# Optimization experiments

Measured on AMD Instinct MI355X. Metric: run time of the kernel, lower is better.

## Reference

```python
import jax, jax.numpy as jnp
import numpy as np

N, E, FEAT, H, C = 50000, 800000, 256, 256, 64
THETA = 0.5


def _l2norm(x, eps=1e-12):
    n = jnp.sqrt(jnp.sum(x * x, axis=-1, keepdims=True))
    return x / jnp.maximum(n, eps)


def _gcn_conv(x, row, col, W, b):
    # x: [N, Fin]; row/col: [E+N] (self loops already appended); all edge weights are 1
    n = x.shape[0]
    h = x @ W                                                   # [N, Fout]
    ones = jnp.ones(row.shape, dtype=h.dtype)
    deg = jax.ops.segment_sum(ones, row, num_segments=n)        # in-degree over rows
    deg_safe = jnp.where(deg > 0, deg, 1.0)
    dinv = jnp.where(deg > 0, jax.lax.rsqrt(deg_safe), 0.0)
    norm = dinv[row] * dinv[col]                                # [E+N]
    msg = norm[:, None] * h[col]                                # gather + weight
    out = jax.ops.segment_sum(msg, row, num_segments=n)         # scatter-add
    return out + b


def setup_inputs() -> dict:
    key = jax.random.key(0)
    ks = jax.random.split(key, 10)
    edge_index = jax.random.randint(ks[0], (2, E), 0, N, dtype=jnp.int32)
    neg_edge_index = jax.random.randint(ks[1], (2, E), 0, N, dtype=jnp.int32)
    features = jax.random.normal(ks[2], (N, FEAT), dtype=jnp.float32)
    label_smoothing = jax.random.uniform(ks[3], (E,), dtype=jnp.float32)
    W1 = jax.random.normal(ks[4], (FEAT, H), dtype=jnp.float32) / np.sqrt(FEAT)
    b1 = jnp.zeros((H,), dtype=jnp.float32)
    W2 = jax.random.normal(ks[5], (H, H), dtype=jnp.float32) / np.sqrt(H)
    b2 = jnp.zeros((H,), dtype=jnp.float32)
    Wy = jax.random.normal(ks[6], (H, C), dtype=jnp.float32) / np.sqrt(H)
    by = jnp.zeros((C,), dtype=jnp.float32)
    return {"edge_index": edge_index, "features": features,
            "label_smoothing": label_smoothing, "neg_edge_index": neg_edge_index,
            "W1": W1, "b1": b1, "W2": W2, "b2": b2, "Wy": Wy, "by": by}


def reference(edge_index, features, label_smoothing, neg_edge_index,
              W1, b1, W2, b2, Wy, by):
    n = features.shape[0]
    self_idx = jnp.arange(n, dtype=edge_index.dtype)
    row = jnp.concatenate([edge_index[0], self_idx])
    col = jnp.concatenate([edge_index[1], self_idx])

    # GCN (dropout=0.0)
    x1 = jax.nn.relu(_gcn_conv(features, row, col, W1, b1))
    x2 = _gcn_conv(x1, row, col, W2, b2)
    rep = _l2norm(x2)
    rep = _l2norm(rep)  # second normalize in q_phi1.forward
    y = rep @ Wy + by

    # reconstruct_loss (i<j filtering done via static-shape masks)
    e0, e1 = edge_index[0], edge_index[1]
    n0, n1 = neg_edge_index[0], neg_edge_index[1]
    pos_mask = (e0 < e1).astype(rep.dtype)
    neg_mask = (n0 < n1).astype(rep.dtype)

    neg_w = jax.nn.relu(jnp.sum(rep[n0] * rep[n1], axis=1))
    pos_w = jax.nn.relu(jnp.sum(rep[e0] * rep[e1], axis=1))
    pos_fsim = jnp.sum(features[e0] * features[e1], axis=1)
    pos = pos_fsim * THETA + pos_w * (1.0 - THETA)

    n_pos = jnp.sum(pos_mask)
    n_neg = jnp.sum(neg_mask)
    neg_loss = jnp.sum(neg_mask * neg_w * neg_w)
    pos_loss = jnp.sum(pos_mask * (pos - label_smoothing) ** 2)
    rec_loss = (neg_loss + pos_loss) * n / (n_neg + n_pos)
    return rep, rec_loss, y
```

## Files before the change

### kernel.cpp

```cpp
#include <hip/hip_runtime.h>
#include <hip/hip_bf16.h>

#define FEAT 256
#define HDIM 256
#define CDIM 64
#define THETA 0.5f
#define APAD 264

typedef float floatx2 __attribute__((ext_vector_type(2)));
typedef __attribute__((ext_vector_type(8))) short bf16x8;
typedef __attribute__((ext_vector_type(4))) float f32x4;

__global__ __launch_bounds__(256) void deg_count(const int* __restrict__ e0, int E, int* deg) {
    int i = blockIdx.x * 256 + threadIdx.x;
    if (i < E) atomicAdd(&deg[e0[i]], 1);
}

__global__ __launch_bounds__(256) void make_dinv(const int* __restrict__ deg, float* __restrict__ dinv, int N) {
    int i = blockIdx.x * 256 + threadIdx.x;
    if (i < N) dinv[i] = rsqrtf((float)(deg[i] + 1));
}

__global__ __launch_bounds__(256) void scan1(const int* __restrict__ deg,
                                             int* __restrict__ rowptr,
                                             int* __restrict__ blkS, int N) {
    __shared__ int sh[256];
    const int tid = threadIdx.x;
    const int i = blockIdx.x * 256 + tid;
    int v = (i < N) ? deg[i] : 0;
    sh[tid] = v;
    __syncthreads();
#pragma unroll
    for (int off = 1; off < 256; off <<= 1) {
        int t = (tid >= off) ? sh[tid - off] : 0;
        __syncthreads();
        sh[tid] += t;
        __syncthreads();
    }
    if (i < N) rowptr[i] = sh[tid] - v;
    if (tid == 255) blkS[blockIdx.x] = sh[255];
}

__global__ __launch_bounds__(256) void scan2(int* __restrict__ blkS, int nb) {
    __shared__ int part[256];
    const int tid = threadIdx.x;
    const int chunk = (nb + 255) / 256;
    const int s = tid * chunk;
    const int e = min(s + chunk, nb);
    int sum = 0;
    for (int i = s; i < e; ++i) sum += blkS[i];
    part[tid] = sum;
    __syncthreads();
#pragma unroll
    for (int off = 1; off < 256; off <<= 1) {
        int t = (tid >= off) ? part[tid - off] : 0;
        __syncthreads();
        part[tid] += t;
        __syncthreads();
    }
    int run = part[tid] - sum;
    for (int i = s; i < e; ++i) {
        int v = blkS[i];
        blkS[i] = run;
        run += v;
    }
}

__global__ __launch_bounds__(256) void scan3(int* __restrict__ rowptr,
                                             int* __restrict__ cursor,
                                             const int* __restrict__ blkS, int N, int E) {
    const int i = blockIdx.x * 256 + threadIdx.x;
    if (i < N) {
        int v = rowptr[i] + blkS[blockIdx.x];
        rowptr[i] = v;
        cursor[i] = v;
    }
    if (i == 0) rowptr[N] = E;
}

__global__ __launch_bounds__(256) void bucket_edges(const int* __restrict__ e0,
                                                    const int* __restrict__ e1,
                                                    int* cursor, int* __restrict__ colIdx, int E) {
    int i = blockIdx.x * 256 + threadIdx.x;
    if (i < E) {
        int r = e0[i];
        int pos = atomicAdd(&cursor[r], 1);
        colIdx[pos] = e1[i];
    }
}

__device__ __forceinline__ unsigned short f2bf(float f) {
    unsigned int u = __float_as_uint(f);
    u += 0x7fffu + ((u >> 16) & 1u);
    return (unsigned short)(u >> 16);
}
__device__ __forceinline__ float bfl(unsigned int u) { return __uint_as_float(u << 16); }
__device__ __forceinline__ float bfh(unsigned int u) { return __uint_as_float(u & 0xffff0000u); }
__device__ __forceinline__ unsigned char f2f8(float f) {
    int w = __builtin_amdgcn_cvt_pk_fp8_f32(f, f, 0, false);
    return (unsigned char)(w & 0xff);
}

__global__ __launch_bounds__(256) void to_fp8(const float* __restrict__ src,
                                              unsigned char* __restrict__ dst, int n8) {
    int i = blockIdx.x * 256 + threadIdx.x;
    if (i >= n8) return;
    float4 a = ((const float4*)src)[2 * i];
    float4 b = ((const float4*)src)[2 * i + 1];
    int w0 = __builtin_amdgcn_cvt_pk_fp8_f32(a.x, a.y, 0, false);
    w0 = __builtin_amdgcn_cvt_pk_fp8_f32(a.z, a.w, w0, true);
    int w1 = __builtin_amdgcn_cvt_pk_fp8_f32(b.x, b.y, 0, false);
    w1 = __builtin_amdgcn_cvt_pk_fp8_f32(b.z, b.w, w1, true);
    uint2 o;
    o.x = (unsigned int)w0;
    o.y = (unsigned int)w1;
    ((uint2*)dst)[i] = o;
}

__global__ __launch_bounds__(256) void transposeW(const float* __restrict__ W,
                                                  unsigned short* __restrict__ Wt) {
    int k = blockIdx.x;
    int n = threadIdx.x;
    Wt[(size_t)n * 256 + k] = f2bf(W[(size_t)k * 256 + n]);
}

__global__ __launch_bounds__(64) void transposeWy(const float* __restrict__ W,
                                                  unsigned short* __restrict__ Wt) {
    int k = blockIdx.x;
    int n = threadIdx.x;
    Wt[(size_t)n * 256 + k] = f2bf(W[(size_t)k * 64 + n]);
}

__device__ __forceinline__ void gemm_core_f8out(const unsigned short* Al,
                                                const unsigned short* __restrict__ Wt,
                                                unsigned char* __restrict__ out,
                                                int m0, int wv, int lane, int M) {
    f32x4 acc[4][4] = {};
    const int r16 = lane & 15;
    const int kg8 = (lane >> 4) * 8;
    const unsigned short* wbase = Wt + ((size_t)(wv * 64 + r16)) * 256 + kg8;
    const unsigned short* abase = Al + r16 * APAD + kg8;

#pragma unroll
    for (int k0 = 0; k0 < 256; k0 += 32) {
        bf16x8 af[4], bfr[4];
#pragma unroll
        for (int mi = 0; mi < 4; ++mi)
            af[mi] = *(const bf16x8*)&abase[mi * 16 * APAD + k0];
#pragma unroll
        for (int ni = 0; ni < 4; ++ni)
            bfr[ni] = *(const bf16x8*)&wbase[ni * 16 * 256 + k0];
#pragma unroll
        for (int mi = 0; mi < 4; ++mi)
#pragma unroll
            for (int ni = 0; ni < 4; ++ni)
                acc[mi][ni] = __builtin_amdgcn_mfma_f32_16x16x32_bf16(af[mi], bfr[ni], acc[mi][ni], 0, 0, 0);
    }

#pragma unroll
    for (int mi = 0; mi < 4; ++mi) {
        int rbase = m0 + mi * 16 + ((lane >> 4) << 2);
#pragma unroll
        for (int ni = 0; ni < 4; ++ni) {
            int col = (wv << 6) + (ni << 4) + (lane & 15);
#pragma unroll
            for (int j = 0; j < 4; ++j) {
                int row = rbase + j;
                if (row < M) out[(size_t)row * 256 + col] = f2f8(acc[mi][ni][j]);
            }
        }
    }
}

__global__ __launch_bounds__(256) void gemm_mfma_f32A(const float* __restrict__ A,
                                                      const unsigned short* __restrict__ Wt,
                                                      unsigned char* __restrict__ out, int M) {
    __shared__ unsigned short Al[64 * APAD];
    const int tid = threadIdx.x;
    const int m0 = blockIdx.x * 64;
#pragma unroll
    for (int i = 0; i < 8; ++i) {
        int u = i * 256 + tid;
        int r = u >> 5;
        int c8 = (u & 31) * 8;
        int row = m0 + r;
        float4 v0, v1;
        if (row < M) {
            v0 = *(const float4*)&A[(size_t)row * 256 + c8];
            v1 = *(const float4*)&A[(size_t)row * 256 + c8 + 4];
        } else {
            v0 = make_float4(0.f, 0.f, 0.f, 0.f);
            v1 = v0;
        }
        uint4 o;
        o.x = (unsigned int)f2bf(v0.x) | ((unsigned int)f2bf(v0.y) << 16);
        o.y = (unsigned int)f2bf(v0.z) | ((unsigned int)f2bf(v0.w) << 16);
        o.z = (unsigned int)f2bf(v1.x) | ((unsigned int)f2bf(v1.y) << 16);
        o.w = (unsigned int)f2bf(v1.z) | ((unsigned int)f2bf(v1.w) << 16);
        *(uint4*)&Al[r * APAD + c8] = o;
    }
    __syncthreads();
    gemm_core_f8out(Al, Wt, out, m0, tid >> 6, tid & 63, M);
}

__global__ __launch_bounds__(256) void gemm_mfma_b16A(const unsigned short* __restrict__ A,
                                                      const unsigned short* __restrict__ Wt,
                                                      unsigned char* __restrict__ out, int M) {
    __shared__ unsigned short Al[64 * APAD];
    const int tid = threadIdx.x;
    const int m0 = blockIdx.x * 64;
#pragma unroll
    for (int i = 0; i < 8; ++i) {
        int u = i * 256 + tid;
        int r = u >> 5;
        int c8 = (u & 31) * 8;
        int row = m0 + r;
        uint4 o = make_uint4(0, 0, 0, 0);
        if (row < M) o = *(const uint4*)&A[(size_t)row * 256 + c8];
        *(uint4*)&Al[r * APAD + c8] = o;
    }
    __syncthreads();
    gemm_core_f8out(Al, Wt, out, m0, tid >> 6, tid & 63, M);
}

__global__ __launch_bounds__(256) void gemm_wy_mfma(const float* __restrict__ A,
                                                    const unsigned short* __restrict__ WyT,
                                                    const float* __restrict__ bias,
                                                    float* __restrict__ out, int M) {
    __shared__ unsigned short Al[64 * APAD];
    const int tid = threadIdx.x;
    const int m0 = blockIdx.x * 64;
    const int wv = tid >> 6;
    const int lane = tid & 63;

#pragma unroll
    for (int i = 0; i < 8; ++i) {
        int u = i * 256 + tid;
        int r = u >> 5;
        int c8 = (u & 31) * 8;
        int row = m0 + r;
        float4 v0, v1;
        if (row < M) {
            v0 = *(const float4*)&A[(size_t)row * 256 + c8];
            v1 = *(const float4*)&A[(size_t)row * 256 + c8 + 4];
        } else {
            v0 = make_float4(0.f, 0.f, 0.f, 0.f);
            v1 = v0;
        }
        uint4 o;
        o.x = (unsigned int)f2bf(v0.x) | ((unsigned int)f2bf(v0.y) << 16);
        o.y = (unsigned int)f2bf(v0.z) | ((unsigned int)f2bf(v0.w) << 16);
        o.z = (unsigned int)f2bf(v1.x) | ((unsigned int)f2bf(v1.y) << 16);
        o.w = (unsigned int)f2bf(v1.z) | ((unsigned int)f2bf(v1.w) << 16);
        *(uint4*)&Al[r * APAD + c8] = o;
    }
    __syncthreads();

    f32x4 acc[4] = {};
    const int r16 = lane & 15;
    const int kg8 = (lane >> 4) * 8;
    const unsigned short* wbase = WyT + ((size_t)(wv * 16 + r16)) * 256 + kg8;
    const unsigned short* abase = Al + r16 * APAD + kg8;

#pragma unroll
    for (int k0 = 0; k0 < 256; k0 += 32) {
        bf16x8 bfr = *(const bf16x8*)&wbase[k0];
#pragma unroll
        for (int mi = 0; mi < 4; ++mi) {
            bf16x8 af = *(const bf16x8*)&abase[mi * 16 * APAD + k0];
            acc[mi] = __builtin_amdgcn_mfma_f32_16x16x32_bf16(af, bfr, acc[mi], 0, 0, 0);
        }
    }

    int col = (wv << 4) + (lane & 15);
    float bv = bias[col];
#pragma unroll
    for (int mi = 0; mi < 4; ++mi) {
        int rbase = m0 + mi * 16 + ((lane >> 4) << 2);
#pragma unroll
        for (int j = 0; j < 4; ++j) {
            int row = rbase + j;
            if (row < M) out[(size_t)row * 64 + col] = acc[mi][j] + bv;
        }
    }
}

template <int DO_NORM>
__global__ __launch_bounds__(256) void spmm_gather_f8(const int* __restrict__ rowptr,
                                                      const int* __restrict__ colIdx,
                                                      const unsigned char* __restrict__ h8,
                                                      const float* __restrict__ dinv,
                                                      const float* __restrict__ bias,
                                                      unsigned short* __restrict__ out_b16,
                                                      float* __restrict__ rep,
                                                      unsigned char* __restrict__ rep8,
                                                      int N) {
    int row = (blockIdx.x * 256 + threadIdx.x) >> 6;
    int lane = threadIdx.x & 63;
    if (row >= N) return;
    int beg = rowptr[row];
    int end = rowptr[row + 1];
    float4 acc = make_float4(0.f, 0.f, 0.f, 0.f);
    int j = beg;
    for (; j + 7 < end; j += 8) {
        int cc[8];
#pragma unroll
        for (int q = 0; q < 8; ++q) cc[q] = colIdx[j + q];
        float ww[8];
#pragma unroll
        for (int q = 0; q < 8; ++q) ww[q] = dinv[cc[q]];
        unsigned int uu[8];
#pragma unroll
        for (int q = 0; q < 8; ++q) uu[q] = *(const unsigned int*)&h8[(size_t)cc[q] * 256 + lane * 4];
#pragma unroll
        for (int q = 0; q < 8; ++q) {
            floatx2 lo = __builtin_amdgcn_cvt_pk_f32_fp8((int)uu[q], false);
            floatx2 hi = __builtin_amdgcn_cvt_pk_f32_fp8((int)uu[q], true);
            acc.x = fmaf(ww[q], lo.x, acc.x); acc.y = fmaf(ww[q], lo.y, acc.y);
            acc.z = fmaf(ww[q], hi.x, acc.z); acc.w = fmaf(ww[q], hi.y, acc.w);
        }
    }
    for (; j < end; ++j) {
        int c = colIdx[j];
        float w = dinv[c];
        unsigned int u = *(const unsigned int*)&h8[(size_t)c * 256 + lane * 4];
        floatx2 lo = __builtin_amdgcn_cvt_pk_f32_fp8((int)u, false);
        floatx2 hi = __builtin_amdgcn_cvt_pk_f32_fp8((int)u, true);
        acc.x = fmaf(w, lo.x, acc.x); acc.y = fmaf(w, lo.y, acc.y);
        acc.z = fmaf(w, hi.x, acc.z); acc.w = fmaf(w, hi.y, acc.w);
    }
    float di = dinv[row];
    float s = di * di;
    unsigned int us = *(const unsigned int*)&h8[(size_t)row * 256 + lane * 4];
    floatx2 slo = __builtin_amdgcn_cvt_pk_f32_fp8((int)us, false);
    floatx2 shi = __builtin_amdgcn_cvt_pk_f32_fp8((int)us, true);
    float4 bv = *(const float4*)&bias[lane * 4];
    float4 r;
    r.x = fmaf(di, acc.x, fmaf(s, slo.x, bv.x));
    r.y = fmaf(di, acc.y, fmaf(s, slo.y, bv.y));
    r.z = fmaf(di, acc.z, fmaf(s, shi.x, bv.z));
    r.w = fmaf(di, acc.w, fmaf(s, shi.y, bv.w));
    if (DO_NORM == 0) {
        r.x = fmaxf(r.x, 0.f);
        r.y = fmaxf(r.y, 0.f);
        r.z = fmaxf(r.z, 0.f);
        r.w = fmaxf(r.w, 0.f);
        uint2 o;
        o.x = (unsigned int)f2bf(r.x) | ((unsigned int)f2bf(r.y) << 16);
        o.y = (unsigned int)f2bf(r.z) | ((unsigned int)f2bf(r.w) << 16);
        *(uint2*)&out_b16[(size_t)row * 256 + lane * 4] = o;
    } else {
        float ss = r.x * r.x + r.y * r.y + r.z * r.z + r.w * r.w;
#pragma unroll
        for (int o = 1; o < 64; o <<= 1) ss += __shfl_xor(ss, o);
        float inv = 1.0f / fmaxf(sqrtf(ss), 1e-12f);
        r.x *= inv; r.y *= inv; r.z *= inv; r.w *= inv;
        float ss2 = r.x * r.x + r.y * r.y + r.z * r.z + r.w * r.w;
#pragma unroll
        for (int o = 1; o < 64; o <<= 1) ss2 += __shfl_xor(ss2, o);
        float inv2 = 1.0f / fmaxf(sqrtf(ss2), 1e-12f);
        r.x *= inv2; r.y *= inv2; r.z *= inv2; r.w *= inv2;
        *(float4*)&rep[(size_t)row * 256 + lane * 4] = r;
        int w = __builtin_amdgcn_cvt_pk_fp8_f32(r.x, r.y, 0, false);
        w = __builtin_amdgcn_cvt_pk_fp8_f32(r.z, r.w, w, true);
        *(unsigned int*)&rep8[(size_t)row * 256 + lane * 4] = (unsigned int)w;
    }
}

__global__ __launch_bounds__(256) void count_blocks(const int* __restrict__ e0,
                                                    const int* __restrict__ e1,
                                                    const int* __restrict__ n0,
                                                    const int* __restrict__ n1,
                                                    int* __restrict__ blkP,
                                                    int* __restrict__ blkN, int E) {
    const int i = blockIdx.x * 256 + threadIdx.x;
    const int lane = threadIdx.x & 63;
    const int w = threadIdx.x >> 6;
    bool vp = false, vn = false;
    if (i < E) {
        vp = e0[i] < e1[i];
        vn = n0[i] < n1[i];
    }
    unsigned long long mp = __ballot(vp);
    unsigned long long mn = __ballot(vn);
    __shared__ int s[8];
    if (lane == 0) {
        s[w] = __popcll(mp);
        s[4 + w] = __popcll(mn);
    }
    __syncthreads();
    if (threadIdx.x == 0) blkP[blockIdx.x] = s[0] + s[1] + s[2] + s[3];
    if (threadIdx.x == 1) blkN[blockIdx.x] = s[4] + s[5] + s[6] + s[7];
}

__global__ __launch_bounds__(256) void scan_blocks(int* __restrict__ blkP, int* __restrict__ blkN,
                                                   int* __restrict__ cnt, int nb) {
    __shared__ int partP[256], partN[256];
    const int tid = threadIdx.x;
    const int chunk = (nb + 255) / 256;
    const int s = tid * chunk;
    const int e = min(s + chunk, nb);
    int sp = 0, sn = 0;
    for (int i = s; i < e; ++i) { sp += blkP[i]; sn += blkN[i]; }
    partP[tid] = sp;
    partN[tid] = sn;
    __syncthreads();
#pragma unroll
    for (int off = 1; off < 256; off <<= 1) {
        int tp = (tid >= off) ? partP[tid - off] : 0;
        int tn = (tid >= off) ? partN[tid - off] : 0;
        __syncthreads();
        partP[tid] += tp;
        partN[tid] += tn;
        __syncthreads();
    }
    int runP = partP[tid] - sp;
    int runN = partN[tid] - sn;
    for (int i = s; i < e; ++i) {
        int vp = blkP[i], vn = blkN[i];
        blkP[i] = runP;
        blkN[i] = runN;
        runP += vp;
        runN += vn;
    }
    if (tid == 255) { cnt[0] = runP; cnt[1] = runN; }
}

__global__ __launch_bounds__(256) void scatter_edges(const int* __restrict__ e0,
                                                     const int* __restrict__ e1,
                                                     const int* __restrict__ n0,
                                                     const int* __restrict__ n1,
                                                     const float* __restrict__ ls,
                                                     const int* __restrict__ blkP,
                                                     const int* __restrict__ blkN,
                                                     int2* __restrict__ posAB,
                                                     float* __restrict__ posLS,
                                                     int2* __restrict__ negCD, int E) {
    const int i = blockIdx.x * 256 + threadIdx.x;
    const int lane = threadIdx.x & 63;
    const int w = threadIdx.x >> 6;
    const unsigned long long below = (lane == 0) ? 0ull : ((1ull << lane) - 1ull);
    int a = 0, b = 0, c = 0, d = 0;
    float lsv = 0.f;
    bool vp = false, vn = false;
    if (i < E) {
        a = e0[i]; b = e1[i];
        c = n0[i]; d = n1[i];
        vp = a < b;
        vn = c < d;
        if (vp) lsv = ls[i];
    }
    unsigned long long mp = __ballot(vp);
    unsigned long long mn = __ballot(vn);
    __shared__ int sP[4], sN[4];
    if (lane == 0) {
        sP[w] = __popcll(mp);
        sN[w] = __popcll(mn);
    }
    __syncthreads();
    int baseP = blkP[blockIdx.x];
    int baseN = blkN[blockIdx.x];
    for (int q = 0; q < 4; ++q) {
        if (q < w) { baseP += sP[q]; baseN += sN[q]; }
    }
    if (vp) {
        int ofs = __popcll(mp & below);
        posAB[baseP + ofs] = make_int2(a, b);
        posLS[baseP + ofs] = lsv;
    }
    if (vn) {
        int ofs = __popcll(mn & below);
        negCD[baseN + ofs] = make_int2(c, d);
    }
}

__device__ __forceinline__ float dot16fp8(uint4 x, uint4 y) {
    float s = 0.f;
    const unsigned int xs[4] = {x.x, x.y, x.z, x.w};
    const unsigned int ys[4] = {y.x, y.y, y.z, y.w};
#pragma unroll
    for (int i = 0; i < 4; ++i) {
        floatx2 xl = __builtin_amdgcn_cvt_pk_f32_fp8((int)xs[i], false);
        floatx2 xh = __builtin_amdgcn_cvt_pk_f32_fp8((int)xs[i], true);
        floatx2 yl = __builtin_amdgcn_cvt_pk_f32_fp8((int)ys[i], false);
        floatx2 yh = __builtin_amdgcn_cvt_pk_f32_fp8((int)ys[i], true);
        s += xl.x * yl.x + xl.y * yl.y + xh.x * yh.x + xh.y * yh.y;
    }
    return s;
}

__global__ __launch_bounds__(256) void loss_pos(const int2* __restrict__ posAB,
                                                const float* __restrict__ posLS,
                                                const int* __restrict__ cnt,
                                                const unsigned char* __restrict__ rep8,
                                                const unsigned char* __restrict__ feat8,
                                                float* accum) {
    const int tid = threadIdx.x;
    const int l8 = tid & 7;
    const int grp = (blockIdx.x * 256 + tid) >> 3;
    const int ngrp = gridDim.x * 32;
    const int P = cnt[0];
    float ap = 0.f;
    for (int e = grp; e < P; e += ngrp) {
        int2 ab = posAB[e];
        const uint4* pra = (const uint4*)&rep8[(size_t)ab.x * 256 + l8 * 32];
        const uint4* prb = (const uint4*)&rep8[(size_t)ab.y * 256 + l8 * 32];
        const uint4* pfa = (const uint4*)&feat8[(size_t)ab.x * 256 + l8 * 32];
        const uint4* pfb = (const uint4*)&feat8[(size_t)ab.y * 256 + l8 * 32];
        uint4 ra0 = pra[0], ra1 = pra[1];
        uint4 rb0 = prb[0], rb1 = prb[1];
        uint4 fa0 = pfa[0], fa1 = pfa[1];
        uint4 fb0 = pfb[0], fb1 = pfb[1];
        float dp = dot16fp8(ra0, rb0) + dot16fp8(ra1, rb1);
        float df = dot16fp8(fa0, fb0) + dot16fp8(fa1, fb1);
#pragma unroll
        for (int o = 1; o < 8; o <<= 1) {
            dp += __shfl_xor(dp, o);
            df += __shfl_xor(df, o);
        }
        if (l8 == 0) {
            float pw = fmaxf(dp, 0.f);
            float pos = THETA * df + (1.0f - THETA) * pw;
            float t = pos - posLS[e];
            ap += t * t;
        }
    }
#pragma unroll
    for (int o = 1; o < 64; o <<= 1) ap += __shfl_xor(ap, o);
    __shared__ float s[4];
    if ((tid & 63) == 0) s[tid >> 6] = ap;
    __syncthreads();
    if (tid == 0) unsafeAtomicAdd(&accum[0], s[0] + s[1] + s[2] + s[3]);
}

__global__ __launch_bounds__(256) void loss_neg(const int2* __restrict__ negCD,
                                                const int* __restrict__ cnt,
                                                const unsigned char* __restrict__ rep8,
                                                float* accum) {
    const int tid = threadIdx.x;
    const int l8 = tid & 7;
    const int grp = (blockIdx.x * 256 + tid) >> 3;
    const int ngrp = gridDim.x * 32;
    const int Q = cnt[1];
    float an = 0.f;
    for (int e = grp; e < Q; e += ngrp) {
        int2 cd = negCD[e];
        const uint4* prc = (const uint4*)&rep8[(size_t)cd.x * 256 + l8 * 32];
        const uint4* prd = (const uint4*)&rep8[(size_t)cd.y * 256 + l8 * 32];
        uint4 rc0 = prc[0], rc1 = prc[1];
        uint4 rd0 = prd[0], rd1 = prd[1];
        float dn = dot16fp8(rc0, rd0) + dot16fp8(rc1, rd1);
#pragma unroll
        for (int o = 1; o < 8; o <<= 1) dn += __shfl_xor(dn, o);
        if (l8 == 0) {
            float nwt = fmaxf(dn, 0.f);
            an += nwt * nwt;
        }
    }
#pragma unroll
    for (int o = 1; o < 64; o <<= 1) an += __shfl_xor(an, o);
    __shared__ float s[4];
    if ((tid & 63) == 0) s[tid >> 6] = an;
    __syncthreads();
    if (tid == 0) unsafeAtomicAdd(&accum[1], s[0] + s[1] + s[2] + s[3]);
}

__global__ void loss_final(const float* __restrict__ accum, const int* __restrict__ cnt,
                           float* __restrict__ out, int N) {
    out[0] = (accum[0] + accum[1]) * (float)N / (float)(cnt[0] + cnt[1]);
}

extern "C" void kernel_launch(void* const* d_in, const int* in_sizes, int n_in,
                              void* d_out, int out_size, void* d_ws, size_t ws_size,
                              hipStream_t stream) {
    const int* edge = (const int*)d_in[0];
    const float* features = (const float*)d_in[1];
    const float* ls = (const float*)d_in[2];
    const int* nedge = (const int*)d_in[3];
    const float* W1 = (const float*)d_in[4];
    const float* b1 = (const float*)d_in[5];
    const float* W2 = (const float*)d_in[6];
    const float* b2 = (const float*)d_in[7];
    const float* Wy = (const float*)d_in[8];
    const float* by = (const float*)d_in[9];

    const int E = in_sizes[0] / 2;
    const int N = in_sizes[1] / FEAT;
    const int* e0 = edge;
    const int* e1 = edge + E;
    const int* n0 = nedge;
    const int* n1 = nedge + E;

    float* rep = (float*)d_out;
    float* rec = rep + (size_t)N * 256;
    float* y = rec + 1;

    char* base = (char*)d_ws;
    size_t off = 0;
    auto carve = [&](size_t bytes) -> void* {
        void* p = base + off;
        off += (bytes + 1023) & ~(size_t)1023;
        return p;
    };
    int* deg = (int*)carve((size_t)N * 4);
    float* dinv = (float*)carve((size_t)N * 4);
    float* accum = (float*)carve(16);
    int* cnt = (int*)carve(16);
    int* rowptr = (int*)carve((size_t)(N + 1) * 4);
    int* cursor = (int*)carve((size_t)N * 4);
    int* colIdx = (int*)carve((size_t)E * 4);
    unsigned char* h8 = (unsigned char*)carve((size_t)N * 256);
    unsigned short* x1B = (unsigned short*)carve((size_t)N * 256 * 2);
    unsigned char* feat8 = (unsigned char*)carve((size_t)N * 256);
    unsigned char* rep8 = (unsigned char*)carve((size_t)N * 256);
    unsigned short* Wt1 = (unsigned short*)carve(256 * 256 * 2);
    unsigned short* Wt2 = (unsigned short*)carve(256 * 256 * 2);
    unsigned short* WyT = (unsigned short*)carve(64 * 256 * 2);
    int2* posAB = (int2*)carve((size_t)E * 8);
    float* posLS = (float*)carve((size_t)E * 4);
    int2* negCD = (int2*)carve((size_t)E * 8);
    const int nb = (E + 255) / 256;
    int* blkP = (int*)carve((size_t)nb * 4);
    int* blkN = (int*)carve((size_t)nb * 4);
    const int nbn = (N + 255) / 256;
    int* blkS = (int*)carve((size_t)nbn * 4);

    hipMemsetAsync(deg, 0, (size_t)N * 4, stream);
    hipMemsetAsync(accum, 0, 16, stream);
    deg_count<<<(E + 255) / 256, 256, 0, stream>>>(e0, E, deg);
    make_dinv<<<(N + 255) / 256, 256, 0, stream>>>(deg, dinv, N);
    scan1<<<nbn, 256, 0, stream>>>(deg, rowptr, blkS, N);
    scan2<<<1, 256, 0, stream>>>(blkS, nbn);
    scan3<<<nbn, 256, 0, stream>>>(rowptr, cursor, blkS, N, E);
    bucket_edges<<<(E + 255) / 256, 256, 0, stream>>>(e0, e1, cursor, colIdx, E);

    count_blocks<<<nb, 256, 0, stream>>>(e0, e1, n0, n1, blkP, blkN, E);
    scan_blocks<<<1, 256, 0, stream>>>(blkP, blkN, cnt, nb);
    scatter_edges<<<nb, 256, 0, stream>>>(e0, e1, n0, n1, ls, blkP, blkN, posAB, posLS, negCD, E);

    const int gblk = (N + 63) / 64;
    const int wblk = (N + 3) / 4;
    const int n8 = N * 256 / 8;

    to_fp8<<<(n8 + 255) / 256, 256, 0, stream>>>(features, feat8, n8);
    transposeW<<<256, 256, 0, stream>>>(W1, Wt1);
    transposeW<<<256, 256, 0, stream>>>(W2, Wt2);
    transposeWy<<<256, 64, 0, stream>>>(Wy, WyT);

    gemm_mfma_f32A<<<gblk, 256, 0, stream>>>(features, Wt1, h8, N);
    spmm_gather_f8<0><<<wblk, 256, 0, stream>>>(rowptr, colIdx, h8, dinv, b1, x1B, nullptr, nullptr, N);

    gemm_mfma_b16A<<<gblk, 256, 0, stream>>>(x1B, Wt2, h8, N);
    spmm_gather_f8<1><<<wblk, 256, 0, stream>>>(rowptr, colIdx, h8, dinv, b2, nullptr, rep, rep8, N);

    gemm_wy_mfma<<<gblk, 256, 0, stream>>>(rep, WyT, by, y, N);

    loss_pos<<<2048, 256, 0, stream>>>(posAB, posLS, cnt, rep8, feat8, accum);
    loss_neg<<<2048, 256, 0, stream>>>(negCD, cnt, rep8, accum);
    loss_final<<<1, 1, 0, stream>>>(accum, cnt, rec, N);
}
```

Before: 405.5 us.

## Fuse preprocessing launches, merge loss kernels, read fp8 rep in Wy GEMM

```diff
diff --git a/kernel.cpp b/kernel.cpp
--- a/kernel.cpp
+++ b/kernel.cpp
@@ -11,23 +11,84 @@
 typedef __attribute__((ext_vector_type(8))) short bf16x8;
 typedef __attribute__((ext_vector_type(4))) float f32x4;
 
-__global__ __launch_bounds__(256) void deg_count(const int* __restrict__ e0, int E, int* deg) {
-    int i = blockIdx.x * 256 + threadIdx.x;
-    if (i < E) atomicAdd(&deg[e0[i]], 1);
-}
-
-__global__ __launch_bounds__(256) void make_dinv(const int* __restrict__ deg, float* __restrict__ dinv, int N) {
-    int i = blockIdx.x * 256 + threadIdx.x;
-    if (i < N) dinv[i] = rsqrtf((float)(deg[i] + 1));
-}
-
-__global__ __launch_bounds__(256) void scan1(const int* __restrict__ deg,
-                                             int* __restrict__ rowptr,
-                                             int* __restrict__ blkS, int N) {
+__device__ __forceinline__ unsigned short f2bf(float f) {
+    unsigned int u = __float_as_uint(f);
+    u += 0x7fffu + ((u >> 16) & 1u);
+    return (unsigned short)(u >> 16);
+}
+__device__ __forceinline__ unsigned char f2f8(float f) {
+    int w = __builtin_amdgcn_cvt_pk_fp8_f32(f, f, 0, false);
+    return (unsigned char)(w & 0xff);
+}
+
+__global__ __launch_bounds__(256) void prep(const int* __restrict__ e0, const int* __restrict__ e1,
+                                            const int* __restrict__ n0, const int* __restrict__ n1,
+                                            int* deg, int* __restrict__ blkP, int* __restrict__ blkN,
+                                            const float* __restrict__ features, unsigned char* __restrict__ feat8,
+                                            const float* __restrict__ W1, unsigned short* __restrict__ Wt1,
+                                            const float* __restrict__ W2, unsigned short* __restrict__ Wt2,
+                                            const float* __restrict__ Wy, unsigned short* __restrict__ WyT,
+                                            int E, int n8, int ebk, int f8bk) {
+    const int b = blockIdx.x;
+    const int tid = threadIdx.x;
+    if (b < ebk) {
+        const int i = b * 256 + tid;
+        const int lane = tid & 63;
+        const int w = tid >> 6;
+        bool vp = false, vn = false;
+        if (i < E) {
+            int a = e0[i], bb = e1[i];
+            atomicAdd(&deg[a], 1);
+            vp = a < bb;
+            vn = n0[i] < n1[i];
+        }
+        unsigned long long mp = __ballot(vp);
+        unsigned long long mn = __ballot(vn);
+        __shared__ int s[8];
+        if (lane == 0) {
+            s[w] = __popcll(mp);
+            s[4 + w] = __popcll(mn);
+        }
+        __syncthreads();
+        if (tid == 0) blkP[b] = s[0] + s[1] + s[2] + s[3];
+        if (tid == 1) blkN[b] = s[4] + s[5] + s[6] + s[7];
+    } else if (b < ebk + f8bk) {
+        int i = (b - ebk) * 256 + tid;
+        if (i < n8) {
+            float4 a = ((const float4*)features)[2 * i];
+            float4 v = ((const float4*)features)[2 * i + 1];
+            int w0 = __builtin_amdgcn_cvt_pk_fp8_f32(a.x, a.y, 0, false);
+            w0 = __builtin_amdgcn_cvt_pk_fp8_f32(a.z, a.w, w0, true);
+            int w1 = __builtin_amdgcn_cvt_pk_fp8_f32(v.x, v.y, 0, false);
+            w1 = __builtin_amdgcn_cvt_pk_fp8_f32(v.z, v.w, w1, true);
+            uint2 o;
+            o.x = (unsigned int)w0;
+            o.y = (unsigned int)w1;
+            ((uint2*)feat8)[i] = o;
+        }
+    } else if (b < ebk + f8bk + 256) {
+        int k = b - ebk - f8bk;
+        Wt1[(size_t)tid * 256 + k] = f2bf(W1[(size_t)k * 256 + tid]);
+    } else if (b < ebk + f8bk + 512) {
+        int k = b - ebk - f8bk - 256;
+        Wt2[(size_t)tid * 256 + k] = f2bf(W2[(size_t)k * 256 + tid]);
+    } else {
+        int b3 = b - ebk - f8bk - 512;
+        int n = tid & 63;
+        int k = b3 * 4 + (tid >> 6);
+        WyT[(size_t)n * 256 + k] = f2bf(Wy[(size_t)k * 64 + n]);
+    }
+}
+
+__global__ __launch_bounds__(256) void scan1_dinv(const int* __restrict__ deg,
+                                                  int* __restrict__ rowptr,
+                                                  int* __restrict__ blkS,
+                                                  float* __restrict__ dinv, int N) {
     __shared__ int sh[256];
     const int tid = threadIdx.x;
     const int i = blockIdx.x * 256 + tid;
     int v = (i < N) ? deg[i] : 0;
+    if (i < N) dinv[i] = rsqrtf((float)(v + 1));
     sh[tid] = v;
     __syncthreads();
 #pragma unroll
@@ -41,41 +102,121 @@
     if (tid == 255) blkS[blockIdx.x] = sh[255];
 }
 
-__global__ __launch_bounds__(256) void scan2(int* __restrict__ blkS, int nb) {
-    __shared__ int part[256];
-    const int tid = threadIdx.x;
-    const int chunk = (nb + 255) / 256;
-    const int s = tid * chunk;
-    const int e = min(s + chunk, nb);
-    int sum = 0;
-    for (int i = s; i < e; ++i) sum += blkS[i];
-    part[tid] = sum;
+__global__ __launch_bounds__(256) void scan2x(int* __restrict__ blkS, int nbn,
+                                              int* __restrict__ blkP, int* __restrict__ blkN,
+                                              int* __restrict__ cnt, int nb) {
+    const int tid = threadIdx.x;
+    if (blockIdx.x == 0) {
+        __shared__ int part[256];
+        const int chunk = (nbn + 255) / 256;
+        const int s = tid * chunk;
+        const int e = min(s + chunk, nbn);
+        int sum = 0;
+        for (int i = s; i < e; ++i) sum += blkS[i];
+        part[tid] = sum;
+        __syncthreads();
+#pragma unroll
+        for (int off = 1; off < 256; off <<= 1) {
+            int t = (tid >= off) ? part[tid - off] : 0;
+            __syncthreads();
+            part[tid] += t;
+            __syncthreads();
+        }
+        int run = part[tid] - sum;
+        for (int i = s; i < e; ++i) {
+            int v = blkS[i];
+            blkS[i] = run;
+            run += v;
+        }
+    } else {
+        __shared__ int partP[256], partN[256];
+        const int chunk = (nb + 255) / 256;
+        const int s = tid * chunk;
+        const int e = min(s + chunk, nb);
+        int sp = 0, sn = 0;
+        for (int i = s; i < e; ++i) { sp += blkP[i]; sn += blkN[i]; }
+        partP[tid] = sp;
+        partN[tid] = sn;
+        __syncthreads();
+#pragma unroll
+        for (int off = 1; off < 256; off <<= 1) {
+            int tp = (tid >= off) ? partP[tid - off] : 0;
+            int tn = (tid >= off) ? partN[tid - off] : 0;
+            __syncthreads();
+            partP[tid] += tp;
+            partN[tid] += tn;
+            __syncthreads();
+        }
+        int runP = partP[tid] - sp;
+        int runN = partN[tid] - sn;
+        for (int i = s; i < e; ++i) {
+            int vp = blkP[i], vn = blkN[i];
+            blkP[i] = runP;
+            blkN[i] = runN;
+            runP += vp;
+            runN += vn;
+        }
+        if (tid == 255) { cnt[0] = runP; cnt[1] = runN; }
+    }
+}
+
+__global__ __launch_bounds__(256) void scan3_scatter(int* __restrict__ rowptr, int* __restrict__ cursor,
+                                                     const int* __restrict__ blkS, int N, int E, int nbn,
+                                                     const int* __restrict__ e0, const int* __restrict__ e1,
+                                                     const int* __restrict__ n0, const int* __restrict__ n1,
+                                                     const float* __restrict__ ls,
+                                                     const int* __restrict__ blkP, const int* __restrict__ blkN,
+                                                     int2* __restrict__ posAB, float* __restrict__ posLS,
+                                                     int2* __restrict__ negCD) {
+    const int b = blockIdx.x;
+    const int tid = threadIdx.x;
+    if (b < nbn) {
+        const int i = b * 256 + tid;
+        if (i < N) {
+            int v = rowptr[i] + blkS[b];
+            rowptr[i] = v;
+            cursor[i] = v;
+        }
+        if (i == 0) rowptr[N] = E;
+        return;
+    }
+    const int eb = b - nbn;
+    const int i = eb * 256 + tid;
+    const int lane = tid & 63;
+    const int w = tid >> 6;
+    const unsigned long long below = (lane == 0) ? 0ull : ((1ull << lane) - 1ull);
+    int a = 0, bb = 0, c = 0, d = 0;
+    float lsv = 0.f;
+    bool vp = false, vn = false;
+    if (i < E) {
+        a = e0[i]; bb = e1[i];
+        c = n0[i]; d = n1[i];
+        vp = a < bb;
+        vn = c < d;
+        if (vp) lsv = ls[i];
+    }
+    unsigned long long mp = __ballot(vp);
+    unsigned long long mn = __ballot(vn);
+    __shared__ int sP[4], sN[4];
+    if (lane == 0) {
+        sP[w] = __popcll(mp);
+        sN[w] = __popcll(mn);
+    }
     __syncthreads();
-#pragma unroll
-    for (int off = 1; off < 256; off <<= 1) {
-        int t = (tid >= off) ? part[tid - off] : 0;
-        __syncthreads();
-        part[tid] += t;
-        __syncthreads();
-    }
-    int run = part[tid] - sum;
-    for (int i = s; i < e; ++i) {
-        int v = blkS[i];
-        blkS[i] = run;
-        run += v;
-    }
-}
-
-__global__ __launch_bounds__(256) void scan3(int* __restrict__ rowptr,
-                                             int* __restrict__ cursor,
-                                             const int* __restrict__ blkS, int N, int E) {
-    const int i = blockIdx.x * 256 + threadIdx.x;
-    if (i < N) {
-        int v = rowptr[i] + blkS[blockIdx.x];
-        rowptr[i] = v;
-        cursor[i] = v;
-    }
-    if (i == 0) rowptr[N] = E;
+    int baseP = blkP[eb];
+    int baseN = blkN[eb];
+    for (int q = 0; q < 4; ++q) {
+        if (q < w) { baseP += sP[q]; baseN += sN[q]; }
+    }
+    if (vp) {
+        int ofs = __popcll(mp & below);
+        posAB[baseP + ofs] = make_int2(a, bb);
+        posLS[baseP + ofs] = lsv;
+    }
+    if (vn) {
+        int ofs = __popcll(mn & below);
+        negCD[baseN + ofs] = make_int2(c, d);
+    }
 }
 
 __global__ __launch_bounds__(256) void bucket_edges(const int* __restrict__ e0,
@@ -87,48 +228,6 @@
         int pos = atomicAdd(&cursor[r], 1);
         colIdx[pos] = e1[i];
     }
-}
-
-__device__ __forceinline__ unsigned short f2bf(float f) {
-    unsigned int u = __float_as_uint(f);
-    u += 0x7fffu + ((u >> 16) & 1u);
-    return (unsigned short)(u >> 16);
-}
-__device__ __forceinline__ float bfl(unsigned int u) { return __uint_as_float(u << 16); }
-__device__ __forceinline__ float bfh(unsigned int u) { return __uint_as_float(u & 0xffff0000u); }
-__device__ __forceinline__ unsigned char f2f8(float f) {
-    int w = __builtin_amdgcn_cvt_pk_fp8_f32(f, f, 0, false);
-    return (unsigned char)(w & 0xff);
-}
-
-__global__ __launch_bounds__(256) void to_fp8(const float* __restrict__ src,
-                                              unsigned char* __restrict__ dst, int n8) {
-    int i = blockIdx.x * 256 + threadIdx.x;
-    if (i >= n8) return;
-    float4 a = ((const float4*)src)[2 * i];
-    float4 b = ((const float4*)src)[2 * i + 1];
-    int w0 = __builtin_amdgcn_cvt_pk_fp8_f32(a.x, a.y, 0, false);
-    w0 = __builtin_amdgcn_cvt_pk_fp8_f32(a.z, a.w, w0, true);
-    int w1 = __builtin_amdgcn_cvt_pk_fp8_f32(b.x, b.y, 0, false);
-    w1 = __builtin_amdgcn_cvt_pk_fp8_f32(b.z, b.w, w1, true);
-    uint2 o;
-    o.x = (unsigned int)w0;
-    o.y = (unsigned int)w1;
-    ((uint2*)dst)[i] = o;
-}
-
-__global__ __launch_bounds__(256) void transposeW(const float* __restrict__ W,
-                                                  unsigned short* __restrict__ Wt) {
-    int k = blockIdx.x;
-    int n = threadIdx.x;
-    Wt[(size_t)n * 256 + k] = f2bf(W[(size_t)k * 256 + n]);
-}
-
-__global__ __launch_bounds__(64) void transposeWy(const float* __restrict__ W,
-                                                  unsigned short* __restrict__ Wt) {
-    int k = blockIdx.x;
-    int n = threadIdx.x;
-    Wt[(size_t)n * 256 + k] = f2bf(W[(size_t)k * 64 + n]);
 }
 
 __device__ __forceinline__ void gemm_core_f8out(const unsigned short* Al,
@@ -223,10 +322,10 @@
     gemm_core_f8out(Al, Wt, out, m0, tid >> 6, tid & 63, M);
 }
 
-__global__ __launch_bounds__(256) void gemm_wy_mfma(const float* __restrict__ A,
-                                                    const unsigned short* __restrict__ WyT,
-                                                    const float* __restrict__ bias,
-                                                    float* __restrict__ out, int M) {
+__global__ __launch_bounds__(256) void gemm_wy_f8A(const unsigned char* __restrict__ rep8,
+                                                   const unsigned short* __restrict__ WyT,
+                                                   const float* __restrict__ bias,
+                                                   float* __restrict__ out, int M) {
     __shared__ unsigned short Al[64 * APAD];
     const int tid = threadIdx.x;
     const int m0 = blockIdx.x * 64;
@@ -234,25 +333,24 @@
     const int lane = tid & 63;
 
 #pragma unroll
-    for (int i = 0; i < 8; ++i) {
+    for (int i = 0; i < 4; ++i) {
         int u = i * 256 + tid;
-        int r = u >> 5;
-        int c8 = (u & 31) * 8;
+        int r = u >> 4;
+        int c16 = (u & 15) * 16;
         int row = m0 + r;
-        float4 v0, v1;
-        if (row < M) {
-            v0 = *(const float4*)&A[(size_t)row * 256 + c8];
-            v1 = *(const float4*)&A[(size_t)row * 256 + c8 + 4];
-        } else {
-            v0 = make_float4(0.f, 0.f, 0.f, 0.f);
-            v1 = v0;
-        }
-        uint4 o;
-        o.x = (unsigned int)f2bf(v0.x) | ((unsigned int)f2bf(v0.y) << 16);
-        o.y = (unsigned int)f2bf(v0.z) | ((unsigned int)f2bf(v0.w) << 16);
-        o.z = (unsigned int)f2bf(v1.x) | ((unsigned int)f2bf(v1.y) << 16);
-        o.w = (unsigned int)f2bf(v1.z) | ((unsigned int)f2bf(v1.w) << 16);
-        *(uint4*)&Al[r * APAD + c8] = o;
+        uint4 v = make_uint4(0, 0, 0, 0);
+        if (row < M) v = *(const uint4*)&rep8[(size_t)row * 256 + c16];
+        unsigned int ws[4] = {v.x, v.y, v.z, v.w};
+        unsigned int ow[8];
+#pragma unroll
+        for (int q = 0; q < 4; ++q) {
+            floatx2 lo = __builtin_amdgcn_cvt_pk_f32_fp8((int)ws[q], false);
+            floatx2 hi = __builtin_amdgcn_cvt_pk_f32_fp8((int)ws[q], true);
+            ow[2 * q] = (unsigned int)f2bf(lo.x) | ((unsigned int)f2bf(lo.y) << 16);
+            ow[2 * q + 1] = (unsigned int)f2bf(hi.x) | ((unsigned int)f2bf(hi.y) << 16);
+        }
+        *(uint4*)&Al[r * APAD + c16] = make_uint4(ow[0], ow[1], ow[2], ow[3]);
+        *(uint4*)&Al[r * APAD + c16 + 8] = make_uint4(ow[4], ow[5], ow[6], ow[7]);
     }
     __syncthreads();
 
@@ -367,113 +465,6 @@
     }
 }
 
-__global__ __launch_bounds__(256) void count_blocks(const int* __restrict__ e0,
-                                                    const int* __restrict__ e1,
-                                                    const int* __restrict__ n0,
-                                                    const int* __restrict__ n1,
-                                                    int* __restrict__ blkP,
-                                                    int* __restrict__ blkN, int E) {
-    const int i = blockIdx.x * 256 + threadIdx.x;
-    const int lane = threadIdx.x & 63;
-    const int w = threadIdx.x >> 6;
-    bool vp = false, vn = false;
-    if (i < E) {
-        vp = e0[i] < e1[i];
-        vn = n0[i] < n1[i];
-    }
-    unsigned long long mp = __ballot(vp);
-    unsigned long long mn = __ballot(vn);
-    __shared__ int s[8];
-    if (lane == 0) {
-        s[w] = __popcll(mp);
-        s[4 + w] = __popcll(mn);
-    }
-    __syncthreads();
-    if (threadIdx.x == 0) blkP[blockIdx.x] = s[0] + s[1] + s[2] + s[3];
-    if (threadIdx.x == 1) blkN[blockIdx.x] = s[4] + s[5] + s[6] + s[7];
-}
-
-__global__ __launch_bounds__(256) void scan_blocks(int* __restrict__ blkP, int* __restrict__ blkN,
-                                                   int* __restrict__ cnt, int nb) {
-    __shared__ int partP[256], partN[256];
-    const int tid = threadIdx.x;
-    const int chunk = (nb + 255) / 256;
-    const int s = tid * chunk;
-    const int e = min(s + chunk, nb);
-    int sp = 0, sn = 0;
-    for (int i = s; i < e; ++i) { sp += blkP[i]; sn += blkN[i]; }
-    partP[tid] = sp;
-    partN[tid] = sn;
-    __syncthreads();
-#pragma unroll
-    for (int off = 1; off < 256; off <<= 1) {
-        int tp = (tid >= off) ? partP[tid - off] : 0;
-        int tn = (tid >= off) ? partN[tid - off] : 0;
-        __syncthreads();
-        partP[tid] += tp;
-        partN[tid] += tn;
-        __syncthreads();
-    }
-    int runP = partP[tid] - sp;
-    int runN = partN[tid] - sn;
-    for (int i = s; i < e; ++i) {
-        int vp = blkP[i], vn = blkN[i];
-        blkP[i] = runP;
-        blkN[i] = runN;
-        runP += vp;
-        runN += vn;
-    }
-    if (tid == 255) { cnt[0] = runP; cnt[1] = runN; }
-}
-
-__global__ __launch_bounds__(256) void scatter_edges(const int* __restrict__ e0,
-                                                     const int* __restrict__ e1,
-                                                     const int* __restrict__ n0,
-                                                     const int* __restrict__ n1,
-                                                     const float* __restrict__ ls,
-                                                     const int* __restrict__ blkP,
-                                                     const int* __restrict__ blkN,
-                                                     int2* __restrict__ posAB,
-                                                     float* __restrict__ posLS,
-                                                     int2* __restrict__ negCD, int E) {
-    const int i = blockIdx.x * 256 + threadIdx.x;
-    const int lane = threadIdx.x & 63;
-    const int w = threadIdx.x >> 6;
-    const unsigned long long below = (lane == 0) ? 0ull : ((1ull << lane) - 1ull);
-    int a = 0, b = 0, c = 0, d = 0;
-    float lsv = 0.f;
-    bool vp = false, vn = false;
-    if (i < E) {
-        a = e0[i]; b = e1[i];
-        c = n0[i]; d = n1[i];
-        vp = a < b;
-        vn = c < d;
-        if (vp) lsv = ls[i];
-    }
-    unsigned long long mp = __ballot(vp);
-    unsigned long long mn = __ballot(vn);
-    __shared__ int sP[4], sN[4];
-    if (lane == 0) {
-        sP[w] = __popcll(mp);
-        sN[w] = __popcll(mn);
-    }
-    __syncthreads();
-    int baseP = blkP[blockIdx.x];
-    int baseN = blkN[blockIdx.x];
-    for (int q = 0; q < 4; ++q) {
-        if (q < w) { baseP += sP[q]; baseN += sN[q]; }
-    }
-    if (vp) {
-        int ofs = __popcll(mp & below);
-        posAB[baseP + ofs] = make_int2(a, b);
-        posLS[baseP + ofs] = lsv;
-    }
-    if (vn) {
-        int ofs = __popcll(mn & below);
-        negCD[baseN + ofs] = make_int2(c, d);
-    }
-}
-
 __device__ __forceinline__ float dot16fp8(uint4 x, uint4 y) {
     float s = 0.f;
     const unsigned int xs[4] = {x.x, x.y, x.z, x.w};
@@ -489,8 +480,9 @@
     return s;
 }
 
-__global__ __launch_bounds__(256) void loss_pos(const int2* __restrict__ posAB,
+__global__ __launch_bounds__(256) void loss_all(const int2* __restrict__ posAB,
                                                 const float* __restrict__ posLS,
+                                                const int2* __restrict__ negCD,
                                                 const int* __restrict__ cnt,
                                                 const unsigned char* __restrict__ rep8,
                                                 const unsigned char* __restrict__ feat8,
@@ -500,69 +492,62 @@
     const int grp = (blockIdx.x * 256 + tid) >> 3;
     const int ngrp = gridDim.x * 32;
     const int P = cnt[0];
-    float ap = 0.f;
-    for (int e = grp; e < P; e += ngrp) {
-        int2 ab = posAB[e];
-        const uint4* pra = (const uint4*)&rep8[(size_t)ab.x * 256 + l8 * 32];
-        const uint4* prb = (const uint4*)&rep8[(size_t)ab.y * 256 + l8 * 32];
-        const uint4* pfa = (const uint4*)&feat8[(size_t)ab.x * 256 + l8 * 32];
-        const uint4* pfb = (const uint4*)&feat8[(size_t)ab.y * 256 + l8 * 32];
-        uint4 ra0 = pra[0], ra1 = pra[1];
-        uint4 rb0 = prb[0], rb1 = prb[1];
-        uint4 fa0 = pfa[0], fa1 = pfa[1];
-        uint4 fb0 = pfb[0], fb1 = pfb[1];
-        float dp = dot16fp8(ra0, rb0) + dot16fp8(ra1, rb1);
-        float df = dot16fp8(fa0, fb0) + dot16fp8(fa1, fb1);
-#pragma unroll
-        for (int o = 1; o < 8; o <<= 1) {
-            dp += __shfl_xor(dp, o);
-            df += __shfl_xor(df, o);
-        }
-        if (l8 == 0) {
-            float pw = fmaxf(dp, 0.f);
-            float pos = THETA * df + (1.0f - THETA) * pw;
-            float t = pos - posLS[e];
-            ap += t * t;
-        }
-    }
-#pragma unroll
-    for (int o = 1; o < 64; o <<= 1) ap += __shfl_xor(ap, o);
-    __shared__ float s[4];
-    if ((tid & 63) == 0) s[tid >> 6] = ap;
+    const int T = P + cnt[1];
+    float ap = 0.f, an = 0.f;
+    for (int g = grp; g < T; g += ngrp) {
+        if (g < P) {
+            int2 ab = posAB[g];
+            const uint4* pra = (const uint4*)&rep8[(size_t)ab.x * 256 + l8 * 32];
+            const uint4* prb = (const uint4*)&rep8[(size_t)ab.y * 256 + l8 * 32];
+            const uint4* pfa = (const uint4*)&feat8[(size_t)ab.x * 256 + l8 * 32];
+            const uint4* pfb = (const uint4*)&feat8[(size_t)ab.y * 256 + l8 * 32];
+            uint4 ra0 = pra[0], ra1 = pra[1];
+            uint4 rb0 = prb[0], rb1 = prb[1];
+            uint4 fa0 = pfa[0], fa1 = pfa[1];
+            uint4 fb0 = pfb[0], fb1 = pfb[1];
+            float dp = dot16fp8(ra0, rb0) + dot16fp8(ra1, rb1);
+            float df = dot16fp8(fa0, fb0) + dot16fp8(fa1, fb1);
+#pragma unroll
+            for (int o = 1; o < 8; o <<= 1) {
+                dp += __shfl_xor(dp, o);
+                df += __shfl_xor(df, o);
+            }
+            if (l8 == 0) {
+                float pw = fmaxf(dp, 0.f);
+                float pos = THETA * df + (1.0f - THETA) * pw;
+                float t = pos - posLS[g];
+                ap += t * t;
+            }
+        } else {
+            int2 cd = negCD[g - P];
+            const uint4* prc = (const uint4*)&rep8[(size_t)cd.x * 256 + l8 * 32];
+            const uint4* prd = (const uint4*)&rep8[(size_t)cd.y * 256 + l8 * 32];
+            uint4 rc0 = prc[0], rc1 = prc[1];
+            uint4 rd0 = prd[0], rd1 = prd[1];
+            float dn = dot16fp8(rc0, rd0) + dot16fp8(rc1, rd1);
+#pragma unroll
+            for (int o = 1; o < 8; o <<= 1) dn += __shfl_xor(dn, o);
+            if (l8 == 0) {
+                float nwt = fmaxf(dn, 0.f);
+                an += nwt * nwt;
+            }
+        }
+    }
+#pragma unroll
+    for (int o = 1; o < 64; o <<= 1) {
+        ap += __shfl_xor(ap, o);
+        an += __shfl_xor(an, o);
+    }
+    __shared__ float s[4][2];
+    if ((tid & 63) == 0) {
+        s[tid >> 6][0] = ap;
+        s[tid >> 6][1] = an;
+    }
     __syncthreads();
-    if (tid == 0) unsafeAtomicAdd(&accum[0], s[0] + s[1] + s[2] + s[3]);
-}
-
-__global__ __launch_bounds__(256) void loss_neg(const int2* __restrict__ negCD,
-                                                const int* __restrict__ cnt,
-                                                const unsigned char* __restrict__ rep8,
-                                                float* accum) {
-    const int tid = threadIdx.x;
-    const int l8 = tid & 7;
-    const int grp = (blockIdx.x * 256 + tid) >> 3;
-    const int ngrp = gridDim.x * 32;
-    const int Q = cnt[1];
-    float an = 0.f;
-    for (int e = grp; e < Q; e += ngrp) {
-        int2 cd = negCD[e];
-        const uint4* prc = (const uint4*)&rep8[(size_t)cd.x * 256 + l8 * 32];
-        const uint4* prd = (const uint4*)&rep8[(size_t)cd.y * 256 + l8 * 32];
-        uint4 rc0 = prc[0], rc1 = prc[1];
-        uint4 rd0 = prd[0], rd1 = prd[1];
-        float dn = dot16fp8(rc0, rd0) + dot16fp8(rc1, rd1);
-#pragma unroll
-        for (int o = 1; o < 8; o <<= 1) dn += __shfl_xor(dn, o);
-        if (l8 == 0) {
-            float nwt = fmaxf(dn, 0.f);
-            an += nwt * nwt;
-        }
-    }
-#pragma unroll
-    for (int o = 1; o < 64; o <<= 1) an += __shfl_xor(an, o);
-    __shared__ float s[4];
-    if ((tid & 63) == 0) s[tid >> 6] = an;
-    __syncthreads();
-    if (tid == 0) unsafeAtomicAdd(&accum[1], s[0] + s[1] + s[2] + s[3]);
+    if (tid == 0) {
+        unsafeAtomicAdd(&accum[0], s[0][0] + s[1][0] + s[2][0] + s[3][0]);
+        unsafeAtomicAdd(&accum[1], s[0][1] + s[1][1] + s[2][1] + s[3][1]);
+    }
 }
 
 __global__ void loss_final(const float* __restrict__ accum, const int* __restrict__ cnt,
@@ -619,33 +604,29 @@
     int2* posAB = (int2*)carve((size_t)E * 8);
     float* posLS = (float*)carve((size_t)E * 4);
     int2* negCD = (int2*)carve((size_t)E * 8);
-    const int nb = (E + 255) / 256;
-    int* blkP = (int*)carve((size_t)nb * 4);
-    int* blkN = (int*)carve((size_t)nb * 4);
+    const int ebk = (E + 255) / 256;
+    int* blkP = (int*)carve((size_t)ebk * 4);
+    int* blkN = (int*)carve((size_t)ebk * 4);
     const int nbn = (N + 255) / 256;
     int* blkS = (int*)carve((size_t)nbn * 4);
 
+    const int n8 = N * 256 / 8;
+    const int f8bk = (n8 + 255) / 256;
+    const int gblk = (N + 63) / 64;
+    const int wblk = (N + 3) / 4;
+
     hipMemsetAsync(deg, 0, (size_t)N * 4, stream);
     hipMemsetAsync(accum, 0, 16, stream);
-    deg_count<<<(E + 255) / 256, 256, 0, stream>>>(e0, E, deg);
-    make_dinv<<<(N + 255) / 256, 256, 0, stream>>>(deg, dinv, N);
-    scan1<<<nbn, 256, 0, stream>>>(deg, rowptr, blkS, N);
-    scan2<<<1, 256, 0, stream>>>(blkS, nbn);
-    scan3<<<nbn, 256, 0, stream>>>(rowptr, cursor, blkS, N, E);
-    bucket_edges<<<(E + 255) / 256, 256, 0, stream>>>(e0, e1, cursor, colIdx, E);
-
-    count_blocks<<<nb, 256, 0, stream>>>(e0, e1, n0, n1, blkP, blkN, E);
-    scan_blocks<<<1, 256, 0, stream>>>(blkP, blkN, cnt, nb);
-    scatter_edges<<<nb, 256, 0, stream>>>(e0, e1, n0, n1, ls, blkP, blkN, posAB, posLS, negCD, E);
-
-    const int gblk = (N + 63) / 64;
-    const int wblk = (N + 3) / 4;
-    const int n8 = N * 256 / 8;
-
-    to_fp8<<<(n8 + 255) / 256, 256, 0, stream>>>(features, feat8, n8);
-    transposeW<<<256, 256, 0, stream>>>(W1, Wt1);
-    transposeW<<<256, 256, 0, stream>>>(W2, Wt2);
-    transposeWy<<<256, 64, 0, stream>>>(Wy, WyT);
+
+    prep<<<ebk + f8bk + 512 + 64, 256, 0, stream>>>(e0, e1, n0, n1, deg, blkP, blkN,
+                                                    features, feat8, W1, Wt1, W2, Wt2, Wy, WyT,
+                                                    E, n8, ebk, f8bk);
+
+    scan1_dinv<<<nbn, 256, 0, stream>>>(deg, rowptr, blkS, dinv, N);
+    scan2x<<<2, 256, 0, stream>>>(blkS, nbn, blkP, blkN, cnt, ebk);
+    scan3_scatter<<<nbn + ebk, 256, 0, stream>>>(rowptr, cursor, blkS, N, E, nbn,
+                                                 e0, e1, n0, n1, ls, blkP, blkN, posAB, posLS, negCD);
+    bucket_edges<<<ebk, 256, 0, stream>>>(e0, e1, cursor, colIdx, E);
 
     gemm_mfma_f32A<<<gblk, 256, 0, stream>>>(features, Wt1, h8, N);
     spmm_gather_f8<0><<<wblk, 256, 0, stream>>>(rowptr, colIdx, h8, dinv, b1, x1B, nullptr, nullptr, N);
@@ -653,9 +634,8 @@
     gemm_mfma_b16A<<<gblk, 256, 0, stream>>>(x1B, Wt2, h8, N);
     spmm_gather_f8<1><<<wblk, 256, 0, stream>>>(rowptr, colIdx, h8, dinv, b2, nullptr, rep, rep8, N);
 
-    gemm_wy_mfma<<<gblk, 256, 0, stream>>>(rep, WyT, by, y, N);
-
-    loss_pos<<<2048, 256, 0, stream>>>(posAB, posLS, cnt, rep8, feat8, accum);
-    loss_neg<<<2048, 256, 0, stream>>>(negCD, cnt, rep8, accum);
+    gemm_wy_f8A<<<gblk, 256, 0, stream>>>(rep8, WyT, by, y, N);
+
+    loss_all<<<2048, 256, 0, stream>>>(posAB, posLS, negCD, cnt, rep8, feat8, accum);
     loss_final<<<1, 1, 0, stream>>>(accum, cnt, rec, N);
 }
```

New measurement: 381.8 us. -5.9%, faster.
